# Kernel optimization log

Measured on AMD Instinct MI355X. Metric: run time of the kernel, lower is better.

The kernel has to match this reference:

```python
import jax, jax.numpy as jnp
import numpy as np

D_MODEL = 1024
N_BLOCK = 20
EPS = 1e-8


def setup_inputs() -> dict:
    key = jax.random.key(0)
    k = jax.random.split(key, 7)
    B, S, D, NB = 8, 2048, D_MODEL, N_BLOCK
    e = jax.random.normal(k[0], (B, S, D), dtype=jnp.float32)
    m = jax.random.normal(k[1], (B, S, D), dtype=jnp.float32)
    state = jax.random.normal(k[2], (1, NB * D), dtype=jnp.float32)
    # learned params of the EntNet-style RNN_cell
    U = jax.random.normal(k[3], (D, D), dtype=jnp.float32) * 0.02
    V = jax.random.normal(k[4], (D, D), dtype=jnp.float32) * 0.02
    W = jax.random.normal(k[5], (D, D), dtype=jnp.float32) * 0.02
    keys = jax.random.normal(k[6], (NB, D), dtype=jnp.float32) * 0.02
    return {"e": e, "m": m, "state": state, "U": U, "V": V, "W": W, "keys": keys}


def reference(e, m, state, U, V, W, keys):
    B, S, D = e.shape
    NB = keys.shape[0]
    h0 = state.reshape(NB, D)  # shared initial memory state across batch
    x = e + m  # combined per-timestep input, (B, S, D)

    def step(h, xt):  # h: (NB, D), xt: (D,)
        # per-slot gate: content similarity + key similarity
        g = jax.nn.sigmoid(h @ xt + keys @ xt)  # (NB,)
        # candidate memory
        cand = jnp.tanh(h @ U.T + keys @ V.T + (W @ xt)[None, :])  # (NB, D)
        h = h + g[:, None] * cand
        # per-slot L2 normalization
        h = h / (jnp.linalg.norm(h, axis=1, keepdims=True) + EPS)
        return h, None

    def run(xseq):  # xseq: (S, D) -> final state (NB, D)
        hT, _ = jax.lax.scan(step, h0, xseq)
        return hT

    out = jax.vmap(run)(x)  # (B, NB, D)
    return out
```

## Files before the change

### kernel.cpp

```cpp
#include <hip/hip_runtime.h>
#include <cstdint>
#include <cstddef>

namespace {

constexpr int D   = 1024;
constexpr int NB  = 20;
constexpr int B   = 8;
constexpr int S   = 2048;
constexpr int NWG = 32;
constexpr float EPS = 1e-8f;

typedef __attribute__((ext_vector_type(4))) float f4_t;
typedef __attribute__((ext_vector_type(8))) short s8_t;
typedef unsigned long long u64_t;

__device__ __forceinline__ unsigned short f2bf(float f) {
  unsigned u = __float_as_uint(f);
  u += 0x7fffu + ((u >> 16) & 1u);
  return (unsigned short)(u >> 16);
}
__device__ __forceinline__ float bf2f(unsigned short h) {
  return __uint_as_float(((unsigned)h) << 16);
}
__device__ __forceinline__ float u64lo(u64_t x) { return __uint_as_float((unsigned)x); }
__device__ __forceinline__ float u64hi(u64_t x) { return __uint_as_float((unsigned)(x >> 32)); }
__device__ __forceinline__ float rcp_f(float x) { return __builtin_amdgcn_rcpf(x); }
__device__ __forceinline__ float sigm_fast(float x) { return rcp_f(1.0f + __expf(-x)); }
__device__ __forceinline__ float tanh_fast(float x) {
  const float e = __expf(2.0f * x);
  return 1.0f - 2.0f * rcp_f(e + 1.0f);
}

#define MFMA(a, b, c) __builtin_amdgcn_mfma_f32_16x16x32_bf16((a), (b), (c), 0, 0, 0)
#define ALOAD64(p) __hip_atomic_load((p), __ATOMIC_RELAXED, __HIP_MEMORY_SCOPE_AGENT)
#define ASTORE64(p, v) __hip_atomic_store((p), (v), __ATOMIC_RELAXED, __HIP_MEMORY_SCOPE_AGENT)
#define ALOAD32(p) __hip_atomic_load((p), __ATOMIC_RELAXED, __HIP_MEMORY_SCOPE_AGENT)
#define ASTORE32(p, v) __hip_atomic_store((p), (v), __ATOMIC_RELAXED, __HIP_MEMORY_SCOPE_AGENT)

constexpr size_t OFF_HBUF = 0;
constexpr size_t OFF_NORM = OFF_HBUF + 2ull * B * NB * 512 * 4;
constexpr size_t OFF_CTR  = OFF_NORM + 2ull * B * NB * NWG * 4;
constexpr size_t OFF_KV   = OFF_CTR + (size_t)B * 32 * 4;
constexpr size_t OFF_KX   = OFF_KV + (size_t)NB * D * 4;
constexpr size_t OFF_UHI  = OFF_KX + (size_t)B * S * NB * 4;
constexpr size_t OFF_ULO  = OFF_UHI + (size_t)D * D * 2;
constexpr size_t OFF_WHI  = OFF_ULO + (size_t)D * D * 2;
constexpr size_t OFF_WLO  = OFF_WHI + (size_t)D * D * 2;


__global__ void k_convert(const float* __restrict__ U, const float* __restrict__ W,
                          unsigned short* __restrict__ Uhi, unsigned short* __restrict__ Ulo,
                          unsigned short* __restrict__ Whi, unsigned short* __restrict__ Wlo) {
  const int n = D * D;
  for (int i = blockIdx.x * blockDim.x + threadIdx.x; i < n; i += gridDim.x * blockDim.x) {
    float u = U[i];
    unsigned short h = f2bf(u);
    Uhi[i] = h;
    Ulo[i] = f2bf(u - bf2f(h));
    float w = W[i];
    h = f2bf(w);
    Whi[i] = h;
    Wlo[i] = f2bf(w - bf2f(h));
  }
}

__global__ void k_kv(const float* __restrict__ keys, const float* __restrict__ V,
                     float* __restrict__ KV) {
  const int tid = threadIdx.x;
  const int j = blockIdx.x * 64 + (tid >> 2);
  const int kq = tid & 3;
  const f4_t* v4 = (const f4_t*)(V + (size_t)j * D + kq * 256);
  const f4_t* k4base = (const f4_t*)keys;
  float acc[NB];
#pragma unroll
  for (int i = 0; i < NB; ++i) acc[i] = 0.f;
  for (int q = 0; q < 64; ++q) {
    const f4_t v = v4[q];
#pragma unroll
    for (int i = 0; i < NB; ++i) {
      const f4_t kk = k4base[i * 256 + kq * 64 + q];
      acc[i] += kk[0] * v[0] + kk[1] * v[1] + kk[2] * v[2] + kk[3] * v[3];
    }
  }
#pragma unroll
  for (int i = 0; i < NB; ++i) {
    float s = acc[i];
    s += __shfl_xor(s, 1);
    s += __shfl_xor(s, 2);
    if (kq == 0) KV[(size_t)i * D + j] = s;
  }
}

__global__ void k_kx(const float* __restrict__ e, const float* __restrict__ m,
                     const float* __restrict__ keys, float* __restrict__ KX) {
  __shared__ f4_t xs[256];
  __shared__ float part[NB][8];
  const int bt = blockIdx.x, tid = threadIdx.x;
  xs[tid] = ((const f4_t*)e)[(size_t)bt * 256 + tid] + ((const f4_t*)m)[(size_t)bt * 256 + tid];
  __syncthreads();
  if (tid < 160) {
    const int i = tid >> 3, s8 = tid & 7;
    float acc = 0.f;
    const f4_t* k4 = (const f4_t*)keys + i * 256 + s8 * 32;
    for (int q = 0; q < 32; ++q) {
      const f4_t kk = k4[q];
      const f4_t xx = xs[s8 * 32 + q];
      acc += kk[0] * xx[0] + kk[1] * xx[1] + kk[2] * xx[2] + kk[3] * xx[3];
    }
    part[i][s8] = acc;
  }
  __syncthreads();
  if (tid < NB) {
    float s = 0.f;
#pragma unroll
    for (int q = 0; q < 8; ++q) s += part[tid][q];
    KX[(size_t)bt * NB + tid] = s;
  }
}

__global__ void k_state(const float* __restrict__ state, unsigned* __restrict__ Hbuf,
                        float* __restrict__ NormP, int* __restrict__ ctr) {
  const int idx = blockIdx.x * 256 + threadIdx.x;
  if (idx < B * NB * 512) {
    const int r = idx % (NB * 512);
    const int i = r >> 9, d2 = (r & 511) << 1;
    const unsigned short a = f2bf(state[i * D + d2]);
    const unsigned short c = f2bf(state[i * D + d2 + 1]);
    Hbuf[idx] = (unsigned)a | ((unsigned)c << 16);
  }
  const int j = idx - B * NB * 512;
  if (j >= 0 && j < B * NB * NWG) NormP[j] = 1.0f / 32.0f;
  const int q = idx - B * NB * 512 - B * NB * NWG;
  if (q >= 0 && q < B * 32) ctr[q] = 0;
}


struct __align__(16) LdsT {
  unsigned short hnA[NB * 1024];
  unsigned short xtA[2][1024];
  float credU[4][2][2][16][20];
  float wxAcc[4][2][16];
  float gAcc[4][2][16];
  float KVs[NB][32];
  float ownH[NB][32];
  float pad_force_1_block_per_cu[3072];
};

__device__ __forceinline__ void build_xt(unsigned short* xt , int tid, f4_t x) {
  const unsigned short h0 = f2bf(x[0]), h1 = f2bf(x[1]), h2 = f2bf(x[2]), h3 = f2bf(x[3]);
  const unsigned short u0 = f2bf(x[0] - bf2f(h0)), u1 = f2bf(x[1] - bf2f(h1));
  const unsigned short u2 = f2bf(x[2] - bf2f(h2)), u3 = f2bf(x[3] - bf2f(h3));
  const int kp = tid << 2;
  *(unsigned*)&xt[kp] = (unsigned)h0 | ((unsigned)h1 << 16);
  *(unsigned*)&xt[kp + 2] = (unsigned)h2 | ((unsigned)h3 << 16);
  *(unsigned*)&xt[1024 + kp] = (unsigned)u0 | ((unsigned)u1 << 16);
  *(unsigned*)&xt[1024 + kp + 2] = (unsigned)u2 | ((unsigned)u3 << 16);
}

__device__ __forceinline__ void stage_h(unsigned short* hn, int tid, const u64_t* hv) {
  const int blkk = tid >> 1;
  const int half = (tid & 1) << 2;
#pragma unroll
  for (int j = 0; j < 20; ++j)
    *(u64_t*)&hn[(j << 10) + ((blkk ^ (j & 15)) << 3) + half] = hv[j];
}

__device__ __forceinline__ void bar_lds() {
  asm volatile("s_waitcnt lgkmcnt(0)\n\ts_barrier" ::: "memory");
}
__device__ __forceinline__ void bar_full() {
  asm volatile("s_waitcnt vmcnt(0) lgkmcnt(0)\n\ts_barrier" ::: "memory");
}

__device__ __forceinline__ void poll32(const unsigned* fb, int ln31, int wg,
                                       unsigned tgt, unsigned pv) {
  if (__ballot(pv >= tgt) == ~0ull) return;
  for (;;) {
    const unsigned v = (ln31 == wg) ? tgt : ALOAD32(fb + ln31);
    if (__ballot(v >= tgt) == ~0ull) return;
    __builtin_amdgcn_s_sleep(1);
  }
}

__launch_bounds__(256, 1)
__global__ void k_rnn(const float* __restrict__ e, const float* __restrict__ m,
                      const float* __restrict__ state,
                      const float* __restrict__ KX, const float* __restrict__ KV,
                      const unsigned short* __restrict__ Uhi, const unsigned short* __restrict__ Ulo,
                      const unsigned short* __restrict__ Whi, const unsigned short* __restrict__ Wlo,
                      unsigned* __restrict__ Hbuf, float* __restrict__ NormP,
                      int* __restrict__ ctr, float* __restrict__ out) {
  __shared__ LdsT L;
  const int tid = threadIdx.x;
  const int b = blockIdx.x >> 5;
  const int wg = blockIdx.x & 31;
  const int wv = tid >> 6;
  const int ln = tid & 63;
  const int l15 = ln & 15;
  const int lo4 = ln >> 4;
  const int ln31 = tid & 31;
  unsigned* ctrp = (unsigned*)ctr + b * 32;

  s8_t BUh[2][8], BUl[2][8], BWh[2][8], BWl[2][8];
  {
    const int rowb = (wg << 5) + l15;
#pragma unroll
    for (int nt = 0; nt < 2; ++nt)
#pragma unroll
      for (int kf = 0; kf < 8; ++kf) {
        const size_t off = (size_t)(rowb + nt * 16) * D + (wv << 8) + (kf << 5) + (lo4 << 3);
        BUh[nt][kf] = *(const s8_t*)(Uhi + off);
        BUl[nt][kf] = *(const s8_t*)(Ulo + off);
        BWh[nt][kf] = *(const s8_t*)(Whi + off);
        BWl[nt][kf] = *(const s8_t*)(Wlo + off);
      }
  }
  if (tid < 160) {
    const int i = tid >> 3, c4 = (tid & 7) << 2;
    *(f4_t*)&L.ownH[i][c4] = *(const f4_t*)(state + (size_t)i * D + (wg << 5) + c4);
    *(f4_t*)&L.KVs[i][c4] = *(const f4_t*)(KV + (size_t)i * D + (wg << 5) + c4);
  }

  f4_t evv, mvv;
  float sreg = 1.f;
  float kxreg = 0.f;

  {
    u64_t hv[20];
    const u64_t* hb8 = (const u64_t*)Hbuf + (size_t)(0 * B + b) * (NB * 256);
#pragma unroll
    for (int j = 0; j < 20; ++j) hv[j] = ALOAD64(hb8 + j * 256 + tid);
    const f4_t x0 = ((const f4_t*)e)[(size_t)(b * S) * 256 + tid] +
                    ((const f4_t*)m)[(size_t)(b * S) * 256 + tid];
    build_xt(&L.xtA[0][0], tid, x0);
    stage_h(L.hnA, tid, hv);
    if (tid < 160) kxreg = KX[(size_t)(b * S) * NB + (tid >> 3)];
    evv = ((const f4_t*)e)[(size_t)(b * S + 1) * 256 + tid];
    mvv = ((const f4_t*)m)[(size_t)(b * S + 1) * 256 + tid];
  }
  __syncthreads();

  for (int t = 0; t < S; ++t) {
    const int nxt2 = (t + 1) & 1;

    f4_t cU00 = {0, 0, 0, 0}, cU01 = {0, 0, 0, 0}, cU10 = {0, 0, 0, 0}, cU11 = {0, 0, 0, 0};
    f4_t cW0 = {0, 0, 0, 0}, cW1 = {0, 0, 0, 0}, cG0 = {0, 0, 0, 0}, cG1 = {0, 0, 0, 0};
    {
      const unsigned short* hb = L.hnA;
      const unsigned short* xb = &L.xtA[0][0];
      const int r1 = 16 + (l15 < 4 ? l15 : 3);
      s8_t A0[8], A1[8], AX[8];
#pragma unroll
      for (int kf = 0; kf < 8; ++kf) {
        const int blk = (wv << 5) + (kf << 2) + lo4;
        A0[kf] = *(const s8_t*)&hb[(l15 << 10) + ((blk ^ l15) << 3)];
        A1[kf] = *(const s8_t*)&hb[(r1 << 10) + ((blk ^ (r1 & 15)) << 3)];
        AX[kf] = *(const s8_t*)&xb[(l15 & 1) * 1024 + (blk << 3)];
      }
#pragma unroll
      for (int kf = 0; kf < 8; ++kf) {
        cU00 = MFMA(A0[kf], BUh[0][kf], cU00);
        cU00 = MFMA(A0[kf], BUl[0][kf], cU00);
        cU01 = MFMA(A0[kf], BUh[1][kf], cU01);
        cU01 = MFMA(A0[kf], BUl[1][kf], cU01);
        cU10 = MFMA(A1[kf], BUh[0][kf], cU10);
        cU10 = MFMA(A1[kf], BUl[0][kf], cU10);
        cU11 = MFMA(A1[kf], BUh[1][kf], cU11);
        cU11 = MFMA(A1[kf], BUl[1][kf], cU11);
        cW0 = MFMA(AX[kf], BWh[0][kf], cW0);
        cW0 = MFMA(AX[kf], BWl[0][kf], cW0);
        cW1 = MFMA(AX[kf], BWh[1][kf], cW1);
        cW1 = MFMA(AX[kf], BWl[1][kf], cW1);
        cG0 = MFMA(AX[kf], A0[kf], cG0);
        cG1 = MFMA(AX[kf], A1[kf], cG1);
      }
    }
#pragma unroll
    for (int q = 0; q < 4; ++q) {
      const int r = (lo4 << 2) + q;
      L.credU[wv][0][0][r][l15] = cU00[q];
      L.credU[wv][0][1][r][l15] = cU01[q];
      L.credU[wv][1][0][r][l15] = cU10[q];
      L.credU[wv][1][1][r][l15] = cU11[q];
    }
    if (lo4 == 0) {
      L.wxAcc[wv][0][l15] = cW0[0] + cW0[1];
      L.wxAcc[wv][1][l15] = cW1[0] + cW1[1];
      L.gAcc[wv][0][l15] = cG0[0] + cG0[1];
      L.gAcc[wv][1][l15] = cG1[0] + cG1[1];
    }
    bar_lds();

    unsigned pv = 0;
    if (t + 1 < S) pv = (ln31 == wg) ? (unsigned)(t + 1) : ALOAD32(ctrp + ln31);

    if (tid < 160) {
      const int i = tid >> 3, c4 = (tid & 7) << 2;
      const int mt = i >> 4, r = i & 15, nt = c4 >> 4, ccc = c4 & 15;
      const f4_t sU = *(const f4_t*)&L.credU[0][mt][nt][r][ccc] +
                      *(const f4_t*)&L.credU[1][mt][nt][r][ccc] +
                      *(const f4_t*)&L.credU[2][mt][nt][r][ccc] +
                      *(const f4_t*)&L.credU[3][mt][nt][r][ccc];
      const f4_t wx = *(const f4_t*)&L.wxAcc[0][nt][ccc] +
                      *(const f4_t*)&L.wxAcc[1][nt][ccc] +
                      *(const f4_t*)&L.wxAcc[2][nt][ccc] +
                      *(const f4_t*)&L.wxAcc[3][nt][ccc];
      const f4_t kv = *(const f4_t*)&L.KVs[i][c4];
      const f4_t oh = *(const f4_t*)&L.ownH[i][c4];
      const float s = sreg;
      const float gpre = s * (L.gAcc[0][mt][r] + L.gAcc[1][mt][r] +
                              L.gAcc[2][mt][r] + L.gAcc[3][mt][r]) + kxreg;
      const float g = sigm_fast(gpre);
      f4_t hn;
      float sq = 0.f;
#pragma unroll
      for (int u = 0; u < 4; ++u) {
        const float cand = tanh_fast(s * sU[u] + kv[u] + wx[u]);
        const float hx = s * oh[u] + g * cand;
        hn[u] = hx;
        sq += hx * hx;
      }
      *(f4_t*)&L.ownH[i][c4] = hn;
      const unsigned d0 = (unsigned)f2bf(hn[0]) | ((unsigned)f2bf(hn[1]) << 16);
      const unsigned d1 = (unsigned)f2bf(hn[2]) | ((unsigned)f2bf(hn[3]) << 16);
      u64_t* hb8 = (u64_t*)Hbuf + (size_t)(nxt2 * B + b) * (NB * 256) +
                   (i << 8) + (wg << 3) + (c4 >> 2);
      ASTORE64(hb8, (u64_t)d0 | ((u64_t)d1 << 32));
      sq += __shfl_xor(sq, 1);
      sq += __shfl_xor(sq, 2);
      sq += __shfl_xor(sq, 4);
      if ((tid & 7) == 0) {
        unsigned* np = (unsigned*)NormP + ((size_t)(nxt2 * B + b) * NB + i) * NWG + wg;
        ASTORE32(np, __float_as_uint(sq));
      }
    }
    bar_full();

    if (tid == 0) ASTORE32(ctrp + wg, (unsigned)(t + 1));

    if (t + 1 < S) {
      poll32(ctrp, ln31, wg, (unsigned)(t + 1), pv);
      u64_t hv[20];
      const u64_t* g0 = (const u64_t*)Hbuf + (size_t)(nxt2 * B + b) * (NB * 256);
#pragma unroll
      for (int j = 0; j < 20; ++j) hv[j] = ALOAD64(g0 + j * 256 + tid);
      float np0 = 0.f;
      if (tid < 160) {
        const int i = tid >> 3;
        const u64_t* n0 = (const u64_t*)NormP + ((size_t)(nxt2 * B + b) * NB + i) * 16 + ((tid & 7) << 1);
        const u64_t a0 = ALOAD64(n0);
        const u64_t a1 = ALOAD64(n0 + 1);
        np0 = u64lo(a0) + u64hi(a0) + u64lo(a1) + u64hi(a1);
        kxreg = KX[((size_t)b * S + t + 1) * NB + i];
      }
      build_xt(&L.xtA[0][0], tid, evv + mvv);
      if (t + 2 < S) {
        evv = ((const f4_t*)e)[(size_t)(b * S + t + 2) * 256 + tid];
        mvv = ((const f4_t*)m)[(size_t)(b * S + t + 2) * 256 + tid];
      }
      stage_h(L.hnA, tid, hv);
      if (tid < 160) {
        float s0 = np0;
        s0 += __shfl_xor(s0, 1);
        s0 += __shfl_xor(s0, 2);
        s0 += __shfl_xor(s0, 4);
        sreg = rcp_f(sqrtf(s0) + EPS);
      }
    }
    asm volatile("s_waitcnt lgkmcnt(0)" ::: "memory");
  }

  poll32(ctrp, ln31, wg, (unsigned)S, 0u);
  if (tid < 160) {
    const int i = tid >> 3, c4 = (tid & 7) << 2;
    const u64_t* np8 = (const u64_t*)NormP + ((size_t)(0 * B + b) * NB + i) * 16 + ((tid & 7) << 1);
    const u64_t x0 = ALOAD64(np8);
    const u64_t x1 = ALOAD64(np8 + 1);
    float sq = u64lo(x0) + u64hi(x0) + u64lo(x1) + u64hi(x1);
    sq += __shfl_xor(sq, 1);
    sq += __shfl_xor(sq, 2);
    sq += __shfl_xor(sq, 4);
    const float sc = rcp_f(sqrtf(sq) + EPS);
    const f4_t oh = *(const f4_t*)&L.ownH[i][c4];
    f4_t ov;
#pragma unroll
    for (int u = 0; u < 4; ++u) ov[u] = sc * oh[u];
    *(f4_t*)(out + (size_t)b * NB * D + (size_t)i * D + (wg << 5) + c4) = ov;
  }
}

}

extern "C" void kernel_launch(void* const* d_in, const int* in_sizes, int n_in,
                              void* d_out, int out_size, void* d_ws, size_t ws_size,
                              hipStream_t stream) {
  const float* e = (const float*)d_in[0];
  const float* m = (const float*)d_in[1];
  const float* state = (const float*)d_in[2];
  const float* U = (const float*)d_in[3];
  const float* V = (const float*)d_in[4];
  const float* W = (const float*)d_in[5];
  const float* keys = (const float*)d_in[6];
  float* out = (float*)d_out;
  char* ws = (char*)d_ws;

  unsigned* Hbuf = (unsigned*)(ws + OFF_HBUF);
  float* NormP = (float*)(ws + OFF_NORM);
  int* ctr = (int*)(ws + OFF_CTR);
  float* KV = (float*)(ws + OFF_KV);
  float* KX = (float*)(ws + OFF_KX);
  unsigned short* Uhi = (unsigned short*)(ws + OFF_UHI);
  unsigned short* Ulo = (unsigned short*)(ws + OFF_ULO);
  unsigned short* Whi = (unsigned short*)(ws + OFF_WHI);
  unsigned short* Wlo = (unsigned short*)(ws + OFF_WLO);

  k_convert<<<512, 256, 0, stream>>>(U, W, Uhi, Ulo, Whi, Wlo);
  k_kv<<<16, 256, 0, stream>>>(keys, V, KV);
  k_kx<<<B * S, 256, 0, stream>>>(e, m, keys, KX);
  k_state<<<342, 256, 0, stream>>>(state, Hbuf, NormP, ctr);
  k_rnn<<<B * NWG, 256, 0, stream>>>(e, m, state, KX, KV, Uhi, Ulo, Whi, Wlo,
                                     Hbuf, NormP, ctr, out);
}
```

Baseline: 11.67 ms.

## Hoist W·x MFMA off the critical path and spread update work across waves

The W·x_t product depends only on the input, not on the recurrent state. It is now computed in the previous iteration's staging phase, overlapping the wait for the cross-workgroup h exchange, instead of inside the per-step critical MFMA chain. The elementwise update threads are also redistributed from the first 160 threads (2.5 waves) to 40 lanes in each of 4 waves, balancing the tail work. This adds register pressure (AX and the W accumulators stay live across the barrier) and an extra LDS wait after build_xt.

```diff
diff --git a/kernel.cpp b/kernel.cpp
--- a/kernel.cpp
+++ b/kernel.cpp
@@ -202,6 +202,10 @@
   const int ln31 = tid & 31;
   unsigned* ctrp = (unsigned*)ctr + b * 32;
 
+  const bool uact = (ln < 40);
+  const int ui = wv * 5 + (ln >> 3);
+  const int uc4 = (ln & 7) << 2;
+
   s8_t BUh[2][8], BUl[2][8], BWh[2][8], BWl[2][8];
   {
     const int rowb = (wg << 5) + l15;
@@ -226,6 +230,9 @@
   float sreg = 1.f;
   float kxreg = 0.f;
 
+  s8_t AX[8];
+  f4_t cWa0 = {0, 0, 0, 0}, cWa1 = {0, 0, 0, 0};
+
   {
     u64_t hv[20];
     const u64_t* hb8 = (const u64_t*)Hbuf + (size_t)(0 * B + b) * (NB * 256);
@@ -235,9 +242,23 @@
                     ((const f4_t*)m)[(size_t)(b * S) * 256 + tid];
     build_xt(&L.xtA[0][0], tid, x0);
     stage_h(L.hnA, tid, hv);
-    if (tid < 160) kxreg = KX[(size_t)(b * S) * NB + (tid >> 3)];
+    if (uact) kxreg = KX[(size_t)(b * S) * NB + ui];
     evv = ((const f4_t*)e)[(size_t)(b * S + 1) * 256 + tid];
     mvv = ((const f4_t*)m)[(size_t)(b * S + 1) * 256 + tid];
+    asm volatile("s_waitcnt lgkmcnt(0)" ::: "memory");
+    const unsigned short* xb = &L.xtA[0][0];
+#pragma unroll
+    for (int kf = 0; kf < 8; ++kf) {
+      const int blk = (wv << 5) + (kf << 2) + lo4;
+      AX[kf] = *(const s8_t*)&xb[(l15 & 1) * 1024 + (blk << 3)];
+    }
+#pragma unroll
+    for (int kf = 0; kf < 8; ++kf) {
+      cWa0 = MFMA(AX[kf], BWh[0][kf], cWa0);
+      cWa0 = MFMA(AX[kf], BWl[0][kf], cWa0);
+      cWa1 = MFMA(AX[kf], BWh[1][kf], cWa1);
+      cWa1 = MFMA(AX[kf], BWl[1][kf], cWa1);
+    }
   }
   __syncthreads();
 
@@ -245,18 +266,16 @@
     const int nxt2 = (t + 1) & 1;
 
     f4_t cU00 = {0, 0, 0, 0}, cU01 = {0, 0, 0, 0}, cU10 = {0, 0, 0, 0}, cU11 = {0, 0, 0, 0};
-    f4_t cW0 = {0, 0, 0, 0}, cW1 = {0, 0, 0, 0}, cG0 = {0, 0, 0, 0}, cG1 = {0, 0, 0, 0};
+    f4_t cG0 = {0, 0, 0, 0}, cG1 = {0, 0, 0, 0};
     {
       const unsigned short* hb = L.hnA;
-      const unsigned short* xb = &L.xtA[0][0];
       const int r1 = 16 + (l15 < 4 ? l15 : 3);
-      s8_t A0[8], A1[8], AX[8];
+      s8_t A0[8], A1[8];
 #pragma unroll
       for (int kf = 0; kf < 8; ++kf) {
         const int blk = (wv << 5) + (kf << 2) + lo4;
         A0[kf] = *(const s8_t*)&hb[(l15 << 10) + ((blk ^ l15) << 3)];
         A1[kf] = *(const s8_t*)&hb[(r1 << 10) + ((blk ^ (r1 & 15)) << 3)];
-        AX[kf] = *(const s8_t*)&xb[(l15 & 1) * 1024 + (blk << 3)];
       }
 #pragma unroll
       for (int kf = 0; kf < 8; ++kf) {
@@ -268,10 +287,6 @@
         cU10 = MFMA(A1[kf], BUl[0][kf], cU10);
         cU11 = MFMA(A1[kf], BUh[1][kf], cU11);
         cU11 = MFMA(A1[kf], BUl[1][kf], cU11);
-        cW0 = MFMA(AX[kf], BWh[0][kf], cW0);
-        cW0 = MFMA(AX[kf], BWl[0][kf], cW0);
-        cW1 = MFMA(AX[kf], BWh[1][kf], cW1);
-        cW1 = MFMA(AX[kf], BWl[1][kf], cW1);
         cG0 = MFMA(AX[kf], A0[kf], cG0);
         cG1 = MFMA(AX[kf], A1[kf], cG1);
       }
@@ -285,8 +300,8 @@
       L.credU[wv][1][1][r][l15] = cU11[q];
     }
     if (lo4 == 0) {
-      L.wxAcc[wv][0][l15] = cW0[0] + cW0[1];
-      L.wxAcc[wv][1][l15] = cW1[0] + cW1[1];
+      L.wxAcc[wv][0][l15] = cWa0[0] + cWa0[1];
+      L.wxAcc[wv][1][l15] = cWa1[0] + cWa1[1];
       L.gAcc[wv][0][l15] = cG0[0] + cG0[1];
       L.gAcc[wv][1][l15] = cG1[0] + cG1[1];
     }
@@ -295,8 +310,8 @@
     unsigned pv = 0;
     if (t + 1 < S) pv = (ln31 == wg) ? (unsigned)(t + 1) : ALOAD32(ctrp + ln31);
 
-    if (tid < 160) {
-      const int i = tid >> 3, c4 = (tid & 7) << 2;
+    if (uact) {
+      const int i = ui, c4 = uc4;
       const int mt = i >> 4, r = i & 15, nt = c4 >> 4, ccc = c4 & 15;
       const f4_t sU = *(const f4_t*)&L.credU[0][mt][nt][r][ccc] +
                       *(const f4_t*)&L.credU[1][mt][nt][r][ccc] +
@@ -330,7 +345,7 @@
       sq += __shfl_xor(sq, 1);
       sq += __shfl_xor(sq, 2);
       sq += __shfl_xor(sq, 4);
-      if ((tid & 7) == 0) {
+      if ((ln & 7) == 0) {
         unsigned* np = (unsigned*)NormP + ((size_t)(nxt2 * B + b) * NB + i) * NWG + wg;
         ASTORE32(np, __float_as_uint(sq));
       }
@@ -346,21 +361,39 @@
 #pragma unroll
       for (int j = 0; j < 20; ++j) hv[j] = ALOAD64(g0 + j * 256 + tid);
       float np0 = 0.f;
-      if (tid < 160) {
-        const int i = tid >> 3;
-        const u64_t* n0 = (const u64_t*)NormP + ((size_t)(nxt2 * B + b) * NB + i) * 16 + ((tid & 7) << 1);
+      if (uact) {
+        const u64_t* n0 = (const u64_t*)NormP + ((size_t)(nxt2 * B + b) * NB + ui) * 16 + ((ln & 7) << 1);
         const u64_t a0 = ALOAD64(n0);
         const u64_t a1 = ALOAD64(n0 + 1);
         np0 = u64lo(a0) + u64hi(a0) + u64lo(a1) + u64hi(a1);
-        kxreg = KX[((size_t)b * S + t + 1) * NB + i];
-      }
+        kxreg = KX[((size_t)b * S + t + 1) * NB + ui];
+      }
+      asm volatile("" ::: "memory");
       build_xt(&L.xtA[0][0], tid, evv + mvv);
+      asm volatile("s_waitcnt lgkmcnt(0)" ::: "memory");
+      {
+        const unsigned short* xb = &L.xtA[0][0];
+#pragma unroll
+        for (int kf = 0; kf < 8; ++kf) {
+          const int blk = (wv << 5) + (kf << 2) + lo4;
+          AX[kf] = *(const s8_t*)&xb[(l15 & 1) * 1024 + (blk << 3)];
+        }
+        cWa0 = (f4_t){0, 0, 0, 0};
+        cWa1 = (f4_t){0, 0, 0, 0};
+#pragma unroll
+        for (int kf = 0; kf < 8; ++kf) {
+          cWa0 = MFMA(AX[kf], BWh[0][kf], cWa0);
+          cWa0 = MFMA(AX[kf], BWl[0][kf], cWa0);
+          cWa1 = MFMA(AX[kf], BWh[1][kf], cWa1);
+          cWa1 = MFMA(AX[kf], BWl[1][kf], cWa1);
+        }
+      }
+      stage_h(L.hnA, tid, hv);
       if (t + 2 < S) {
         evv = ((const f4_t*)e)[(size_t)(b * S + t + 2) * 256 + tid];
         mvv = ((const f4_t*)m)[(size_t)(b * S + t + 2) * 256 + tid];
       }
-      stage_h(L.hnA, tid, hv);
-      if (tid < 160) {
+      if (uact) {
         float s0 = np0;
         s0 += __shfl_xor(s0, 1);
         s0 += __shfl_xor(s0, 2);
@@ -372,9 +405,9 @@
   }
 
   poll32(ctrp, ln31, wg, (unsigned)S, 0u);
-  if (tid < 160) {
-    const int i = tid >> 3, c4 = (tid & 7) << 2;
-    const u64_t* np8 = (const u64_t*)NormP + ((size_t)(0 * B + b) * NB + i) * 16 + ((tid & 7) << 1);
+  if (uact) {
+    const int i = ui, c4 = uc4;
+    const u64_t* np8 = (const u64_t*)NormP + ((size_t)(0 * B + b) * NB + i) * 16 + ((ln & 7) << 1);
     const u64_t x0 = ALOAD64(np8);
     const u64_t x1 = ALOAD64(np8 + 1);
     float sq = u64lo(x0) + u64hi(x0) + u64lo(x1) + u64hi(x1);
```

New measurement: 11.37 ms. 1.03x faster.
